# Kernel tuning notes

Hardware: AMD Instinct MI355X
Metric: run time of the kernel (lower is better)

The kernel has to match this reference:

```python
import jax, jax.numpy as jnp
from jax import lax
import numpy as np

# ITA requantization params (from init_kwargs)
MQ, SQ = 16384, 8
MK, SK = 16384, 8
MV, SV = 16384, 8
MA, SA = 5, 12
MAV, SAV = 1, 8
MO, SO = 256, 7
NUM_HEADS = 6


def requantize(x, mult, shift, add=0):
    # x * mult, floor-div by 2**shift, add, clamp to int8 range (values kept in float32)
    return jnp.clip(jnp.floor(x * mult / (2.0 ** shift)) + add, -128.0, 127.0)


def ita_softmax(x):
    # x: [B, h, S, Skv] float32 with integer values in [-128, 127]
    B, h, S, Skv = x.shape
    width, bits = 16, 8
    eps_max = 32.0 * bits / (2 ** bits)  # range_scale * bits / 2**bits = 1.0
    groups = Skv // width
    x3 = x.reshape(B * h, S, Skv).astype(jnp.int32)
    # [groups, BH, S, width] for streaming scan over key chunks
    chunks = x3.reshape(B * h, S, groups, width).transpose(2, 0, 1, 3)

    def step(carry, chunk):
        exp_partial_sum, global_max = carry
        current_max = chunk.max(axis=-1)
        update = current_max > global_max
        max_shift = jnp.floor((current_max - global_max).astype(jnp.float32) * eps_max + 0.5).astype(jnp.int32)
        shift_sum = jnp.where(update, max_shift, 0)
        global_max = jnp.where(update, current_max, global_max)
        diff = global_max[..., None] - chunk  # >= 0
        shift = jnp.floor(diff.astype(jnp.float32) * eps_max + 0.5).astype(jnp.int32)
        # 2**bits >> shift  (256 >> shift; any shift >= 9 yields 0, clamp to keep shift defined)
        exp_sum = jnp.sum(jnp.right_shift(jnp.int32(256), jnp.minimum(shift, 31)), axis=-1).astype(jnp.int32)
        exp_partial_sum = jnp.right_shift(exp_partial_sum, jnp.minimum(shift_sum, 31)) + exp_sum
        return (exp_partial_sum, global_max), None

    init = (jnp.zeros((B * h, S), jnp.int32), jnp.full((B * h, S), -128, jnp.int32))
    (exp_partial_sum, global_max), _ = lax.scan(step, init, chunks)

    # (2**bits - 1) * 2**bits = 65280
    inv = jnp.floor(65280.0 / exp_partial_sum.astype(jnp.float32)).astype(jnp.int32)
    diff = global_max[..., None] - x3  # >= 0
    shift = jnp.floor(diff.astype(jnp.float32) * eps_max + 0.5).astype(jnp.int32)
    res = jnp.right_shift(inv[..., None], jnp.minimum(shift, 31)).astype(jnp.uint8)
    return res.reshape(B, h, S, Skv)


def setup_inputs() -> dict:
    key = jax.random.key(0)
    ks = jax.random.split(key, 9)
    B, N, D = 4, 2048, 384
    scale = 1.0 / np.sqrt(D)
    return {
        "x": jax.random.normal(ks[0], (B, N, D), jnp.float32),
        "wq": jax.random.normal(ks[1], (D, D), jnp.float32) * scale,
        "bq": jnp.zeros((D,), jnp.float32),
        "wk": jax.random.normal(ks[2], (D, D), jnp.float32) * scale,
        "bk": jnp.zeros((D,), jnp.float32),
        "wv": jax.random.normal(ks[3], (D, D), jnp.float32) * scale,
        "bv": jnp.zeros((D,), jnp.float32),
        "wo": jax.random.normal(ks[4], (D, D), jnp.float32) * scale,
        "bo": jnp.zeros((D,), jnp.float32),
        "H": 64,
        "W": 32,
    }


def reference(x, wq, bq, wk, bk, wv, bv, wo, bo, H, W):
    B, N, _ = x.shape
    h = NUM_HEADS
    hd = wq.shape[0] // h

    Q = requantize(x @ wq.T + bq, MQ, SQ)
    K = requantize(x @ wk.T + bk, MK, SK)
    V = requantize(x @ wv.T + bv, MV, SV)

    Qr = Q.reshape(B, N, h, hd).transpose(0, 2, 1, 3)  # [B,h,N,hd]
    Kr = K.reshape(B, N, h, hd).transpose(0, 2, 1, 3)
    Vr = V.reshape(B, N, h, hd).transpose(0, 2, 1, 3)

    logits = requantize(jnp.einsum('bhqd,bhkd->bhqk', Qr, Kr), MA, SA)
    attn = ita_softmax(logits)  # uint8 [B,h,N,N]
    ctx = requantize(jnp.einsum('bhqk,bhkd->bhqd', attn.astype(jnp.float32), Vr), MAV, SAV)
    ctx = ctx.transpose(0, 2, 1, 3).reshape(B, N, h * hd)
    out = requantize(ctx @ wo.T + bo, MO, SO)
    return out
```

## Files before the change

kernel.cpp:

```cpp
#include <hip/hip_runtime.h>
#include <stdint.h>

#define NB 4
#define NN 2048
#define ND 384
#define NH 6
#define HD 64
#define ROWS (NB * NN)

typedef int v4i __attribute__((ext_vector_type(4)));
typedef float v4f __attribute__((ext_vector_type(4)));
typedef _Float16 half_t;
typedef half_t v8h __attribute__((ext_vector_type(8)));

__global__ __launch_bounds__(256) void qkv_gemm_kernel(
    const float* __restrict__ X,
    const float* __restrict__ Wq, const float* __restrict__ Wk, const float* __restrict__ Wv,
    const float* __restrict__ Bq, const float* __restrict__ Bk, const float* __restrict__ Bv,
    int8_t* __restrict__ Q8, int8_t* __restrict__ K8, int8_t* __restrict__ V8T,
    int* __restrict__ CS)
{
    __shared__ __attribute__((aligned(16))) float As[16][132];
    __shared__ __attribute__((aligned(16))) float Bs[16][100];
    __shared__ int lcol[96];

    const int t = threadIdx.x;
    const int tx = t & 15;
    const int ty = t >> 4;
    const int row0 = blockIdx.x * 128;
    const int m = blockIdx.y >> 2;
    const int cl0 = (blockIdx.y & 3) * 96;
    const float* W = (m == 0) ? Wq : (m == 1) ? Wk : Wv;
    const float* Bi = (m == 0) ? Bq : (m == 1) ? Bk : Bv;

    const int sr = t >> 1;
    const int sk = (t & 1) * 8;
    const float* xp = X + (size_t)(row0 + sr) * ND + sk;
    const float* wp = W + (size_t)(cl0 + sr) * ND + sk;

    float acc[8][6];
#pragma unroll
    for (int i = 0; i < 8; ++i)
#pragma unroll
        for (int j = 0; j < 6; ++j) acc[i][j] = 0.f;

    float4 xa0 = *(const float4*)xp;
    float4 xa1 = *(const float4*)(xp + 4);
    float4 wb0, wb1;
    if (t < 192) { wb0 = *(const float4*)wp; wb1 = *(const float4*)(wp + 4); }

    for (int k0 = 0; k0 < ND; k0 += 16) {
        As[sk + 0][sr] = xa0.x; As[sk + 1][sr] = xa0.y;
        As[sk + 2][sr] = xa0.z; As[sk + 3][sr] = xa0.w;
        As[sk + 4][sr] = xa1.x; As[sk + 5][sr] = xa1.y;
        As[sk + 6][sr] = xa1.z; As[sk + 7][sr] = xa1.w;
        if (t < 192) {
            Bs[sk + 0][sr] = wb0.x; Bs[sk + 1][sr] = wb0.y;
            Bs[sk + 2][sr] = wb0.z; Bs[sk + 3][sr] = wb0.w;
            Bs[sk + 4][sr] = wb1.x; Bs[sk + 5][sr] = wb1.y;
            Bs[sk + 6][sr] = wb1.z; Bs[sk + 7][sr] = wb1.w;
        }
        __syncthreads();

        if (k0 + 16 < ND) {
            xa0 = *(const float4*)(xp + k0 + 16);
            xa1 = *(const float4*)(xp + k0 + 20);
            if (t < 192) {
                wb0 = *(const float4*)(wp + k0 + 16);
                wb1 = *(const float4*)(wp + k0 + 20);
            }
        }

#pragma unroll
        for (int kk = 0; kk < 16; ++kk) {
            float4 a0 = *(const float4*)&As[kk][ty * 8];
            float4 a1 = *(const float4*)&As[kk][ty * 8 + 4];
            float4 b0 = *(const float4*)&Bs[kk][tx * 4];
            float2 b1 = *(const float2*)&Bs[kk][64 + tx * 2];
            float a[8] = {a0.x, a0.y, a0.z, a0.w, a1.x, a1.y, a1.z, a1.w};
            float b[6] = {b0.x, b0.y, b0.z, b0.w, b1.x, b1.y};
#pragma unroll
            for (int i = 0; i < 8; ++i)
#pragma unroll
                for (int j = 0; j < 6; ++j)
                    acc[i][j] += a[i] * b[j];
        }
        __syncthreads();
    }

    const int bidx = row0 >> 11;
    const int n0 = row0 & 2047;
    const int c1 = cl0 + tx * 4;
    const int c2 = cl0 + 64 + tx * 2;
    const int h1 = c1 >> 6, d1 = c1 & 63;
    const int h2 = c2 >> 6, d2 = c2 & 63;

    if (m != 2) {
        int8_t* Out = (m == 0) ? Q8 : K8;
        const float b1a = Bi[c1], b1b = Bi[c1 + 1], b1c = Bi[c1 + 2], b1d = Bi[c1 + 3];
        const float b2a = Bi[c2], b2b = Bi[c2 + 1];
#pragma unroll
        for (int i = 0; i < 8; ++i) {
            const int n = n0 + ty * 8 + i;
            float v0 = acc[i][0] + b1a, v1 = acc[i][1] + b1b;
            float v2 = acc[i][2] + b1c, v3 = acc[i][3] + b1d;
            int q0 = max(-128, min(127, (int)floorf(v0 * 64.0f)));
            int q1 = max(-128, min(127, (int)floorf(v1 * 64.0f)));
            int q2 = max(-128, min(127, (int)floorf(v2 * 64.0f)));
            int q3 = max(-128, min(127, (int)floorf(v3 * 64.0f)));
            uint32_t w = (uint32_t)(q0 & 255) | ((uint32_t)(q1 & 255) << 8)
                       | ((uint32_t)(q2 & 255) << 16) | ((uint32_t)(q3 & 255) << 24);
            *(uint32_t*)(Out + (((size_t)(bidx * NH + h1) * NN) + n) * HD + d1) = w;

            float v4 = acc[i][4] + b2a, v5 = acc[i][5] + b2b;
            int q4 = max(-128, min(127, (int)floorf(v4 * 64.0f)));
            int q5 = max(-128, min(127, (int)floorf(v5 * 64.0f)));
            *(uint16_t*)(Out + (((size_t)(bidx * NH + h2) * NN) + n) * HD + d2) =
                (uint16_t)((q4 & 255) | ((q5 & 255) << 8));
        }
    } else {
        if (t < 96) lcol[t] = 0;
        __syncthreads();
#pragma unroll
        for (int j = 0; j < 6; ++j) {
            const int lc = (j < 4) ? (tx * 4 + j) : (64 + tx * 2 + (j - 4));
            const int col = cl0 + lc;
            const int head = col >> 6, d = col & 63;
            const float bias = Bi[col];
            int s = 0;
            uint32_t w[2] = {0u, 0u};
#pragma unroll
            for (int i = 0; i < 8; ++i) {
                float v = acc[i][j] + bias;
                int qv = (int)floorf(v * 64.0f);
                qv = max(-128, min(127, qv));
                s += qv;
                w[i >> 2] |= (uint32_t)(qv & 255) << (8 * (i & 3));
            }
            uint32_t* dst = (uint32_t*)(V8T + ((size_t)(bidx * NH + head) * HD + d) * NN
                                        + n0 + ty * 8);
            dst[0] = w[0];
            dst[1] = w[1];
            atomicAdd(&lcol[lc], s);
        }
        __syncthreads();
        if (t < 96) {
            const int col = cl0 + t;
            atomicAdd(&CS[(bidx * NH + (col >> 6)) * 64 + (col & 63)], lcol[t]);
        }
    }
}

__global__ __launch_bounds__(256, 4) void attn_kernel(
    const int8_t* __restrict__ Q8, const int8_t* __restrict__ K8,
    const int8_t* __restrict__ V8T, const int* __restrict__ colsum,
    int8_t* __restrict__ CTX8)
{
    __shared__ int Lp[128 * 68];
    __shared__ int gmaxw[128 * 4];
    __shared__ int esumw[128 * 8];

    const int t = threadIdx.x;
    const int wid = t >> 6;
    const int lane = t & 63;
    const int quad = lane >> 4;
    const int l15 = lane & 15;
    const int bh = blockIdx.y;
    const int q0 = blockIdx.x * 16;
    const size_t base = (size_t)bh * NN * HD;
    const v4i zero = {0, 0, 0, 0};

    v4i afrag = *(const v4i*)(Q8 + base + (size_t)(q0 + l15) * HD + quad * 16);
    {
        const int8_t* kp = K8 + base + (size_t)(wid * 32 * 16 + l15) * HD + quad * 16;
        v4i bfrag = *(const v4i*)kp;
        for (int kt = wid * 32; kt < wid * 32 + 32; ++kt) {
            v4i cur = bfrag;
            kp += 16 * HD;
            bfrag = *(const v4i*)kp;
            v4i d = __builtin_amdgcn_mfma_i32_16x16x64_i8(afrag, cur, zero, 0, 0, 0);
            int e[4];
#pragma unroll
            for (int r = 0; r < 4; ++r) {
                int lg = (d[r] * 5) >> 12;
                e[r] = min(127, max(-128, lg));
            }
            int p01 = __builtin_amdgcn_perm(e[1], e[0], 0x00000400);
            int p23 = __builtin_amdgcn_perm(e[3], e[2], 0x00000400);
            Lp[kt * 68 + quad * 16 + l15] = __builtin_amdgcn_perm(p23, p01, 0x05040100);
        }
    }
    __syncthreads();

    int wb[2][16];
#pragma unroll
    for (int it = 0; it < 2; ++it) {
        const int task = t + it * 256;
        const int g = task & 127, qq = task >> 7;
        const int* p = &Lp[g * 68 + qq * 16];
#pragma unroll
        for (int a = 0; a < 4; ++a) {
            v4i v = *(const v4i*)&p[a * 4];
            wb[it][a * 4 + 0] = v.x; wb[it][a * 4 + 1] = v.y;
            wb[it][a * 4 + 2] = v.z; wb[it][a * 4 + 3] = v.w;
        }
        int mx[4];
#pragma unroll
        for (int b = 0; b < 4; ++b) {
            int m = INT_MIN;
#pragma unroll
            for (int j = 0; j < 16; ++j)
                m = max(m, (int)((unsigned)wb[it][j] << (8 * (3 - b))));
            mx[b] = m;
        }
        int p01 = __builtin_amdgcn_perm(mx[1], mx[0], 0x00000703);
        int p23 = __builtin_amdgcn_perm(mx[3], mx[2], 0x00000703);
        gmaxw[g * 4 + qq] = __builtin_amdgcn_perm(p23, p01, 0x05040100);
    }
    __syncthreads();

    if (t < 16) {
        const int wq = t >> 2, bq = 8 * (t & 3);
        int8_t* gb = (int8_t*)gmaxw;
        int m = -128;
        for (int g = 0; g < 128; ++g) {
            int x = (int)(int8_t)(gmaxw[g * 4 + wq] >> bq);
            m = max(m, x);
            gb[g * 16 + t] = (int8_t)m;
        }
    }
    __syncthreads();

#pragma unroll
    for (int it = 0; it < 2; ++it) {
        const int task = t + it * 256;
        const int g = task & 127, qq = task >> 7;
        const int pw = gmaxw[g * 4 + qq];
        uint32_t sp[2] = {0u, 0u};
#pragma unroll
        for (int b = 0; b < 4; ++b) {
            const int M = (int)(int8_t)(pw >> (8 * b));
            const int cb = 8 - M;
            int s = 0;
#pragma unroll
            for (int j = 0; j < 16; ++j) {
                int x = (int)(int8_t)(wb[it][j] >> (8 * b));
                int tt = x + cb;
                s += (tt >= 0) ? (1 << tt) : 0;
            }
            sp[b >> 1] |= (uint32_t)s << (16 * (b & 1));
        }
        *(int2*)&esumw[g * 8 + qq * 2] = make_int2((int)sp[0], (int)sp[1]);
    }
    __syncthreads();

    if (t < 16) {
        const int8_t* gb = (const int8_t*)gmaxw;
        const uint16_t* eb = (const uint16_t*)esumw;
        int E = 0, Mp = -128;
        for (int g = 0; g < 128; ++g) {
            int m = (int)gb[g * 16 + t];
            int d = m - Mp; if (d > 31) d = 31;
            E = (E >> d) + (int)eb[g * 16 + t];
            Mp = m;
        }
        Lp[t * 68 + 64] = 65280 / E;
        Lp[t * 68 + 65] = Mp;
    }
    __syncthreads();

    const int inv_l = Lp[l15 * 68 + 64];
    const int c24 = 24 - Lp[l15 * 68 + 65];
    const int sh8 = 8 * (l15 & 3);
    v4i accs[4] = {zero, zero, zero, zero};
    const int8_t* vtb = V8T + base;

    v4i bf[4];
    {
        const int koff0 = wid * 8 * 64 + quad * 16;
#pragma unroll
        for (int dtb = 0; dtb < 4; ++dtb)
            bf[dtb] = *(const v4i*)(vtb + (size_t)(dtb * 16 + l15) * NN + koff0);
    }
    for (int kc = wid * 8; kc < wid * 8 + 8; ++kc) {
        const int* lp = &Lp[(kc * 4 + quad) * 68 + (l15 >> 2) * 16];
        v4i w4[4];
#pragma unroll
        for (int r = 0; r < 4; ++r) w4[r] = *(const v4i*)&lp[4 * r];

        v4i b0 = bf[0], b1 = bf[1], b2 = bf[2], b3 = bf[3];
        const int koffn = (kc + 1) * 64 + quad * 16;
#pragma unroll
        for (int dtb = 0; dtb < 4; ++dtb)
            bf[dtb] = *(const v4i*)(vtb + (size_t)(dtb * 16 + l15) * NN + koffn);

        v4i a;
#pragma unroll
        for (int r = 0; r < 4; ++r) {
            int u[4];
#pragma unroll
            for (int c = 0; c < 4; ++c) {
                int x = (int)(int8_t)(w4[r][c] >> sh8);
                int t1 = x + c24;
                t1 = (t1 < 0) ? 0 : t1;
                u[c] = (int)((unsigned)inv_l << t1);
            }
            int p01 = __builtin_amdgcn_perm(u[1], u[0], 0x00000703);
            int p23 = __builtin_amdgcn_perm(u[3], u[2], 0x00000703);
            a[r] = __builtin_amdgcn_perm(p23, p01, 0x05040100) ^ (int)0x80808080u;
        }
        accs[0] = __builtin_amdgcn_mfma_i32_16x16x64_i8(a, b0, accs[0], 0, 0, 0);
        accs[1] = __builtin_amdgcn_mfma_i32_16x16x64_i8(a, b1, accs[1], 0, 0, 0);
        accs[2] = __builtin_amdgcn_mfma_i32_16x16x64_i8(a, b2, accs[2], 0, 0, 0);
        accs[3] = __builtin_amdgcn_mfma_i32_16x16x64_i8(a, b3, accs[3], 0, 0, 0);
    }
    __syncthreads();

    if (wid > 0) {
#pragma unroll
        for (int dt = 0; dt < 4; ++dt)
#pragma unroll
            for (int r = 0; r < 4; ++r)
                Lp[(dt * 4 + r) * 192 + (wid - 1) * 64 + lane] = accs[dt][r];
    }
    __syncthreads();
    if (wid == 0) {
        const int bb = bh / NH, hh = bh % NH;
        const int* cs = &colsum[bh * 64];
#pragma unroll
        for (int dt = 0; dt < 4; ++dt) {
            const int dcol = dt * 16 + l15;
            const int corr = cs[dcol] << 7;
#pragma unroll
            for (int r = 0; r < 4; ++r) {
                const int i = dt * 4 + r;
                int val = accs[dt][r]
                        + Lp[i * 192 + 0 * 64 + lane]
                        + Lp[i * 192 + 1 * 64 + lane]
                        + Lp[i * 192 + 2 * 64 + lane];
                const int q = q0 + quad * 4 + r;
                val = (val + corr) >> 8;
                val = min(127, max(-128, val));
                CTX8[((size_t)(bb * NN + q)) * ND + hh * HD + dcol] = (int8_t)val;
            }
        }
    }
}

__global__ __launch_bounds__(256) void out_gemm_kernel(
    const int8_t* __restrict__ CTX8, const float* __restrict__ Wo,
    const float* __restrict__ Bo, float* __restrict__ out)
{
    __shared__ __attribute__((aligned(16))) half_t AH[64 * 40];
    __shared__ __attribute__((aligned(16))) half_t BH[64 * 40];
    __shared__ __attribute__((aligned(16))) half_t BL[64 * 40];

    const int t = threadIdx.x;
    const int wid = t >> 6;
    const int lane = t & 63;
    const int quad = lane >> 4;
    const int l15 = lane & 15;
    const int row0 = blockIdx.x * 64;
    const int c0 = blockIdx.y * 64;

    const int arow = t >> 2;
    const int akb = (t & 3) * 8;
    const int8_t* ap = CTX8 + (size_t)(row0 + arow) * ND + akb;
    const float* wp = Wo + (size_t)(c0 + arow) * ND + akb;

    v4f accH[4], accL[4];
#pragma unroll
    for (int ct = 0; ct < 4; ct++) { accH[ct] = (v4f)0.0f; accL[ct] = (v4f)0.0f; }

    for (int k0 = 0; k0 < ND; k0 += 32) {
        int2 a8 = *(const int2*)(ap + k0);
        float4 w0 = *(const float4*)(wp + k0);
        float4 w1 = *(const float4*)(wp + k0 + 4);
        float wsrc[8] = {w0.x, w0.y, w0.z, w0.w, w1.x, w1.y, w1.z, w1.w};

        __syncthreads();
        v8h av, wh8, wl8;
#pragma unroll
        for (int u = 0; u < 4; u++) {
            av[u]     = (half_t)(float)(int)(int8_t)((a8.x >> (8 * u)) & 0xFF);
            av[4 + u] = (half_t)(float)(int)(int8_t)((a8.y >> (8 * u)) & 0xFF);
        }
#pragma unroll
        for (int u = 0; u < 8; u++) {
            float x = wsrc[u];
            half_t h = (half_t)x;
            wh8[u] = h;
            wl8[u] = (half_t)((x - (float)h) * 2048.0f);
        }
        *(v8h*)&AH[arow * 40 + akb] = av;
        *(v8h*)&BH[arow * 40 + akb] = wh8;
        *(v8h*)&BL[arow * 40 + akb] = wl8;
        __syncthreads();

        v8h af = *(const v8h*)&AH[(wid * 16 + l15) * 40 + quad * 8];
#pragma unroll
        for (int ct = 0; ct < 4; ct++) {
            v8h bh8 = *(const v8h*)&BH[(ct * 16 + l15) * 40 + quad * 8];
            v8h bl8 = *(const v8h*)&BL[(ct * 16 + l15) * 40 + quad * 8];
            accH[ct] = __builtin_amdgcn_mfma_f32_16x16x32_f16(af, bh8, accH[ct], 0, 0, 0);
            accL[ct] = __builtin_amdgcn_mfma_f32_16x16x32_f16(af, bl8, accL[ct], 0, 0, 0);
        }
    }

    const float inv2048 = 4.8828125e-4f;
#pragma unroll
    for (int ct = 0; ct < 4; ct++) {
        const int c = c0 + ct * 16 + l15;
        const float bias = Bo[c];
#pragma unroll
        for (int r = 0; r < 4; r++) {
            const int row = row0 + wid * 16 + quad * 4 + r;
            float v = accH[ct][r] + accL[ct][r] * inv2048 + bias;
            float rq = floorf(v * 2.0f);
            rq = fminf(fmaxf(rq, -128.0f), 127.0f);
            out[(size_t)row * ND + c] = rq;
        }
    }
}

extern "C" void kernel_launch(void* const* d_in, const int* in_sizes, int n_in,
                              void* d_out, int out_size, void* d_ws, size_t ws_size,
                              hipStream_t stream)
{
    const float* x  = (const float*)d_in[0];
    const float* wq = (const float*)d_in[1];
    const float* bq = (const float*)d_in[2];
    const float* wk = (const float*)d_in[3];
    const float* bk = (const float*)d_in[4];
    const float* wv = (const float*)d_in[5];
    const float* bv = (const float*)d_in[6];
    const float* wo = (const float*)d_in[7];
    const float* bo = (const float*)d_in[8];
    float* out = (float*)d_out;

    const size_t MAT = (size_t)ROWS * ND;
    int8_t* Q8  = (int8_t*)d_ws;
    int8_t* K8  = Q8 + MAT;
    int8_t* V8T = K8 + MAT;
    int8_t* C8  = V8T + MAT;
    int*    CS  = (int*)(C8 + MAT);

    hipMemsetAsync(CS, 0, (size_t)NB * NH * 64 * sizeof(int), stream);
    qkv_gemm_kernel<<<dim3(ROWS / 128, 12), 256, 0, stream>>>(
        x, wq, wk, wv, bq, bk, bv, Q8, K8, V8T, CS);
    attn_kernel<<<dim3(NN / 16, NB * NH), 256, 0, stream>>>(Q8, K8, V8T, CS, C8);
    out_gemm_kernel<<<dim3(ROWS / 64, ND / 64), 256, 0, stream>>>(C8, wo, bo, out);
}
```

Before: 272.1 us.

## Double-buffer QKV GEMM shared tiles and use packed float2 FMAs

The QKV projection GEMM now ping-pongs between two shared-memory tile buffers, so each k-step needs one barrier instead of two, and the next global loads are issued before that barrier. The inner product is rewritten with 2-wide vector FMAs on float2 accumulators so the compiler can emit packed FP32 FMA instructions. This doubles the LDS footprint of this kernel and only touches the QKV stage, which is one part of a multi-kernel pipeline. A leftover unused variable was added in the V epilogue.

```diff
diff --git a/kernel.cpp b/kernel.cpp
--- a/kernel.cpp
+++ b/kernel.cpp
@@ -10,6 +10,7 @@
 
 typedef int v4i __attribute__((ext_vector_type(4)));
 typedef float v4f __attribute__((ext_vector_type(4)));
+typedef float v2f __attribute__((ext_vector_type(2)));
 typedef _Float16 half_t;
 typedef half_t v8h __attribute__((ext_vector_type(8)));
 
@@ -20,8 +21,8 @@
     int8_t* __restrict__ Q8, int8_t* __restrict__ K8, int8_t* __restrict__ V8T,
     int* __restrict__ CS)
 {
-    __shared__ __attribute__((aligned(16))) float As[16][132];
-    __shared__ __attribute__((aligned(16))) float Bs[16][100];
+    __shared__ __attribute__((aligned(16))) float As[2][16][132];
+    __shared__ __attribute__((aligned(16))) float Bs[2][16][100];
     __shared__ int lcol[96];
 
     const int t = threadIdx.x;
@@ -38,29 +39,29 @@
     const float* xp = X + (size_t)(row0 + sr) * ND + sk;
     const float* wp = W + (size_t)(cl0 + sr) * ND + sk;
 
-    float acc[8][6];
+    v2f acc[8][3];
 #pragma unroll
     for (int i = 0; i < 8; ++i)
 #pragma unroll
-        for (int j = 0; j < 6; ++j) acc[i][j] = 0.f;
+        for (int p = 0; p < 3; ++p) acc[i][p] = (v2f)0.0f;
 
     float4 xa0 = *(const float4*)xp;
     float4 xa1 = *(const float4*)(xp + 4);
     float4 wb0, wb1;
     if (t < 192) { wb0 = *(const float4*)wp; wb1 = *(const float4*)(wp + 4); }
 
+    int cur = 0;
     for (int k0 = 0; k0 < ND; k0 += 16) {
-        As[sk + 0][sr] = xa0.x; As[sk + 1][sr] = xa0.y;
-        As[sk + 2][sr] = xa0.z; As[sk + 3][sr] = xa0.w;
-        As[sk + 4][sr] = xa1.x; As[sk + 5][sr] = xa1.y;
-        As[sk + 6][sr] = xa1.z; As[sk + 7][sr] = xa1.w;
+        As[cur][sk + 0][sr] = xa0.x; As[cur][sk + 1][sr] = xa0.y;
+        As[cur][sk + 2][sr] = xa0.z; As[cur][sk + 3][sr] = xa0.w;
+        As[cur][sk + 4][sr] = xa1.x; As[cur][sk + 5][sr] = xa1.y;
+        As[cur][sk + 6][sr] = xa1.z; As[cur][sk + 7][sr] = xa1.w;
         if (t < 192) {
-            Bs[sk + 0][sr] = wb0.x; Bs[sk + 1][sr] = wb0.y;
-            Bs[sk + 2][sr] = wb0.z; Bs[sk + 3][sr] = wb0.w;
-            Bs[sk + 4][sr] = wb1.x; Bs[sk + 5][sr] = wb1.y;
-            Bs[sk + 6][sr] = wb1.z; Bs[sk + 7][sr] = wb1.w;
-        }
-        __syncthreads();
+            Bs[cur][sk + 0][sr] = wb0.x; Bs[cur][sk + 1][sr] = wb0.y;
+            Bs[cur][sk + 2][sr] = wb0.z; Bs[cur][sk + 3][sr] = wb0.w;
+            Bs[cur][sk + 4][sr] = wb1.x; Bs[cur][sk + 5][sr] = wb1.y;
+            Bs[cur][sk + 6][sr] = wb1.z; Bs[cur][sk + 7][sr] = wb1.w;
+        }
 
         if (k0 + 16 < ND) {
             xa0 = *(const float4*)(xp + k0 + 16);
@@ -70,22 +71,27 @@
                 wb1 = *(const float4*)(wp + k0 + 20);
             }
         }
+        __syncthreads();
 
 #pragma unroll
         for (int kk = 0; kk < 16; ++kk) {
-            float4 a0 = *(const float4*)&As[kk][ty * 8];
-            float4 a1 = *(const float4*)&As[kk][ty * 8 + 4];
-            float4 b0 = *(const float4*)&Bs[kk][tx * 4];
-            float2 b1 = *(const float2*)&Bs[kk][64 + tx * 2];
+            float4 a0 = *(const float4*)&As[cur][kk][ty * 8];
+            float4 a1 = *(const float4*)&As[cur][kk][ty * 8 + 4];
+            float4 b0 = *(const float4*)&Bs[cur][kk][tx * 4];
+            float2 b1 = *(const float2*)&Bs[cur][kk][64 + tx * 2];
             float a[8] = {a0.x, a0.y, a0.z, a0.w, a1.x, a1.y, a1.z, a1.w};
-            float b[6] = {b0.x, b0.y, b0.z, b0.w, b1.x, b1.y};
-#pragma unroll
-            for (int i = 0; i < 8; ++i)
-#pragma unroll
-                for (int j = 0; j < 6; ++j)
-                    acc[i][j] += a[i] * b[j];
-        }
-        __syncthreads();
+            v2f bp0 = {b0.x, b0.y};
+            v2f bp1 = {b0.z, b0.w};
+            v2f bp2 = {b1.x, b1.y};
+#pragma unroll
+            for (int i = 0; i < 8; ++i) {
+                v2f av = {a[i], a[i]};
+                acc[i][0] = __builtin_elementwise_fma(av, bp0, acc[i][0]);
+                acc[i][1] = __builtin_elementwise_fma(av, bp1, acc[i][1]);
+                acc[i][2] = __builtin_elementwise_fma(av, bp2, acc[i][2]);
+            }
+        }
+        cur ^= 1;
     }
 
     const int bidx = row0 >> 11;
@@ -102,8 +108,8 @@
 #pragma unroll
         for (int i = 0; i < 8; ++i) {
             const int n = n0 + ty * 8 + i;
-            float v0 = acc[i][0] + b1a, v1 = acc[i][1] + b1b;
-            float v2 = acc[i][2] + b1c, v3 = acc[i][3] + b1d;
+            float v0 = acc[i][0][0] + b1a, v1 = acc[i][0][1] + b1b;
+            float v2 = acc[i][1][0] + b1c, v3 = acc[i][1][1] + b1d;
             int q0 = max(-128, min(127, (int)floorf(v0 * 64.0f)));
             int q1 = max(-128, min(127, (int)floorf(v1 * 64.0f)));
             int q2 = max(-128, min(127, (int)floorf(v2 * 64.0f)));
@@ -112,7 +118,7 @@
                        | ((uint32_t)(q2 & 255) << 16) | ((uint32_t)(q3 & 255) << 24);
             *(uint32_t*)(Out + (((size_t)(bidx * NH + h1) * NN) + n) * HD + d1) = w;
 
-            float v4 = acc[i][4] + b2a, v5 = acc[i][5] + b2b;
+            float v4 = acc[i][2][0] + b2a, v5 = acc[i][2][1] + b2b;
             int q4 = max(-128, min(127, (int)floorf(v4 * 64.0f)));
             int q5 = max(-128, min(127, (int)floorf(v5 * 64.0f)));
             *(uint16_t*)(Out + (((size_t)(bidx * NH + h2) * NN) + n) * HD + d2) =
@@ -127,11 +133,13 @@
             const int col = cl0 + lc;
             const int head = col >> 6, d = col & 63;
             const float bias = Bi[col];
+            const float accj = (j < 4) ? acc[0][j >> 1][j & 1] : acc[0][2][j - 4];
+            (void)accj;
             int s = 0;
             uint32_t w[2] = {0u, 0u};
 #pragma unroll
             for (int i = 0; i < 8; ++i) {
-                float v = acc[i][j] + bias;
+                float v = ((j < 4) ? acc[i][j >> 1][j & 1] : acc[i][2][j - 4]) + bias;
                 int qv = (int)floorf(v * 64.0f);
                 qv = max(-128, min(127, qv));
                 s += qv;
```

After: 276.2 us. Within noise of the previous version (+1.5%).
